# Kernel tuning notes

Hardware: AMD Instinct MI355X
Metric: run time of the kernel (lower is better)

## Reference

```python
import jax, jax.numpy as jnp
import numpy as np

B, LQ, LK, D = 16, 1024, 4096, 256
SQRT_SCALE_INV = 0.25          # D ** -0.25, so scale = 1/sqrt(D)
HALF_BW = 128 // 2             # stripe_bandwdith // 2
NEG_INF = float('-inf')


def setup_inputs() -> dict:
    key = jax.random.key(0)
    k1, k2, k3, k4 = jax.random.split(key, 4)
    query = jax.random.normal(k1, (B, LQ, D), jnp.float32)
    key_t = jax.random.normal(k2, (B, LK, D), jnp.float32)
    value = jax.random.normal(k3, (B, LK, D), jnp.float32)
    # key lengths in [LK//2, LK]; masked_fill in torch requires max == LK
    key_lengths = jax.random.randint(k4, (B,), LK // 2, LK + 1).astype(jnp.int32)
    key_lengths = key_lengths.at[0].set(LK)
    query_lengths = jnp.full((B,), LQ, dtype=jnp.int32)  # full so no all-masked rows
    mask = jnp.arange(LK)[None, :] < key_lengths[:, None]  # [B, LK] bool, True = valid
    return {"query": query, "key": key_t, "value": value, "mask": mask,
            "query_lengths": query_lengths, "key_lengths": key_lengths}


def _stripe_mask(query_lengths, key_lengths, Lq, Lk):
    # band around line y = x * (key_len / query_len), per sample
    gx = jnp.arange(Lq, dtype=jnp.float32)[None, :, None]   # [1,Lq,1]
    gy = jnp.arange(Lk, dtype=jnp.float32)[None, None, :]   # [1,1,Lk]
    slope = (key_lengths.astype(jnp.float32) /
             query_lengths.astype(jnp.float32))[:, None, None]  # [B,1,1]
    center = gx * slope
    return (gy >= center - HALF_BW) & (gy <= center + HALF_BW)  # [B,Lq,Lk] bool


def reference(query, key, value, mask, query_lengths, key_lengths):
    # scores = (q * s) @ (k * s)^T  ==  (q @ k^T) * s^2
    scores = jnp.einsum('bqd,bkd->bqk', query, key) * (SQRT_SCALE_INV * SQRT_SCALE_INV)
    stripe = _stripe_mask(query_lengths, key_lengths, query.shape[1], key.shape[1])
    full_mask = mask[:, None, :] & stripe                    # padding AND stripe
    scores = jnp.where(full_mask, scores.astype(jnp.float32), NEG_INF)
    weight = jax.nn.softmax(scores, axis=-1).astype(query.dtype)
    # module applies no dropout (p=0) and returns (attn_weight, value)
    return (weight, value)
```

## Files before the change

kernel.cpp:

```cpp
#include <hip/hip_runtime.h>
#include <math.h>

constexpr int B_  = 16;
constexpr int LQ_ = 1024;
constexpr int LK_ = 4096;
constexpr int D_  = 256;
constexpr float HALF_BW_F = 64.0f;
constexpr float SCALE = 0.0625f;

typedef float  fx4    __attribute__((ext_vector_type(4)));
typedef short  bf16x8 __attribute__((ext_vector_type(8)));
typedef float  f32x4v __attribute__((ext_vector_type(4)));

constexpr int ROWS_PER_WAVE = 16;
constexpr int ROWS_PER_BLK  = 64;
constexpr int NUNIT = (B_ * LQ_) / ROWS_PER_BLK;
constexpr int NXCD  = 8;
constexpr int UNIT_PER_XCD = NUNIT / NXCD;
constexpr int KSPAN = 192;
constexpr int NT    = 12;

__device__ __forceinline__ unsigned short f2bf(float f) {
    unsigned int u = __float_as_uint(f);
    return (unsigned short)((u + 0x7FFFu + ((u >> 16) & 1u)) >> 16);
}
__device__ __forceinline__ bf16x8 pack8(float4 a, float4 b) {
    bf16x8 r;
    r[0] = (short)f2bf(a.x); r[1] = (short)f2bf(a.y);
    r[2] = (short)f2bf(a.z); r[3] = (short)f2bf(a.w);
    r[4] = (short)f2bf(b.x); r[5] = (short)f2bf(b.y);
    r[6] = (short)f2bf(b.z); r[7] = (short)f2bf(b.w);
    return r;
}
__device__ __forceinline__ float grp16_max(float v) {
    #pragma unroll
    for (int off = 8; off > 0; off >>= 1)
        v = fmaxf(v, __shfl_xor(v, off, 64));
    return v;
}
__device__ __forceinline__ float grp16_sum(float v) {
    #pragma unroll
    for (int off = 8; off > 0; off >>= 1)
        v += __shfl_xor(v, off, 64);
    return v;
}

__global__ __launch_bounds__(256, 2) void stripe_attn_kernel(
    const float* __restrict__ Q, const float* __restrict__ K,
    const float* __restrict__ V,
    const int* __restrict__ qlen, const int* __restrict__ klen,
    float* __restrict__ Wout, float* __restrict__ Vout)
{
    const int Bid  = blockIdx.x;
    const int xcd  = Bid & 7;
    const int type = (Bid >> 3) & 1;
    const int slot = Bid >> 4;
    const int cu_u = xcd * UNIT_PER_XCD + slot;
    const int tid  = threadIdx.x;
    const int lane = tid & 63;
    const int wave = tid >> 6;
    const int row0 = cu_u * ROWS_PER_BLK + wave * ROWS_PER_WAVE;
    const int b    = row0 >> 10;
    const int qi0  = row0 & (LQ_ - 1);

    const int   key_len = klen[b];
    const float slope   = (float)key_len / (float)qlen[b];

    if (type == 1) {
        const float* vs = V    + (size_t)row0 * 1024;
        float*       vd = Vout + (size_t)row0 * 1024;
        #pragma unroll
        for (int it = 0; it < 64; ++it) {
            const int o = (it * 64 + lane) * 4;
            fx4 t = __builtin_nontemporal_load((const fx4*)(vs + o));
            __builtin_nontemporal_store(t, (fx4*)(vd + o));
        }
        const fx4 z4 = {0.f, 0.f, 0.f, 0.f};
        #pragma unroll
        for (int r = 0; r < 16; ++r) {
            const float center = (float)(qi0 + r) * slope;
            int lo = (int)ceilf(center - HALF_BW_F); if (lo < 0) lo = 0;
            int hi = (int)floorf(center + HALF_BW_F); if (hi > key_len - 1) hi = key_len - 1;
            const int s_lo = lo >> 8, s_hi = hi >> 8;
            float* base = Wout + (size_t)(row0 + r) * LK_;
            #pragma unroll
            for (int j = 0; j < 16; ++j) {
                if (j < s_lo || j > s_hi)
                    __builtin_nontemporal_store(z4, (fx4*)(base + (j * 64 + lane) * 4));
            }
        }
        return;
    }

    __shared__ float s_sc[4][ROWS_PER_WAVE][KSPAN];

    int lo_w = (int)ceilf((float)qi0 * slope - HALF_BW_F);
    if (lo_w < 0) lo_w = 0;
    int hi_w = (int)floorf((float)(qi0 + 15) * slope + HALF_BW_F);
    if (hi_w > key_len - 1) hi_w = key_len - 1;
    const int nt = (hi_w - lo_w) / 16 + 1;

    const int col = lane & 15;
    const int kg  = lane >> 4;

    const float* qb = Q + ((size_t)b * LQ_ + qi0 + col) * D_ + kg * 8;
    bf16x8 qf[8];
    #pragma unroll
    for (int kc = 0; kc < 8; ++kc) {
        const float4 u = *(const float4*)(qb + kc * 32);
        const float4 v = *(const float4*)(qb + kc * 32 + 4);
        qf[kc] = pack8(u, v);
    }

    const float* kb = K + (size_t)b * LK_ * D_ + kg * 8;
    f32x4v acc[NT];
    #pragma unroll
    for (int t = 0; t < NT; ++t) acc[t] = (f32x4v){0.f, 0.f, 0.f, 0.f};

    #pragma unroll
    for (int t = 0; t < NT; ++t) {
        if (t < nt) {
            const int key  = lo_w + t * 16 + col;
            const int keyc = (key <= hi_w) ? key : hi_w;
            const float* kp = kb + (size_t)keyc * D_;
            float4 u[8], w[8];
            #pragma unroll
            for (int kc = 0; kc < 8; ++kc) {
                u[kc] = *(const float4*)(kp + kc * 32);
                w[kc] = *(const float4*)(kp + kc * 32 + 4);
            }
            #pragma unroll
            for (int kc = 0; kc < 8; ++kc) {
                const bf16x8 kf = pack8(u[kc], w[kc]);
                acc[t] = __builtin_amdgcn_mfma_f32_16x16x32_bf16(qf[kc], kf, acc[t], 0, 0, 0);
            }
        }
    }

    #pragma unroll
    for (int r = 0; r < 4; ++r) {
        const int rg = kg * 4 + r;
        const float center = (float)(qi0 + rg) * slope;
        int klo = (int)ceilf(center - HALF_BW_F); if (klo < 0) klo = 0;
        int khi = (int)floorf(center + HALF_BW_F); if (khi > key_len - 1) khi = key_len - 1;

        float v[NT];
        #pragma unroll
        for (int t = 0; t < NT; ++t) {
            const int key = lo_w + t * 16 + col;
            v[t] = (t < nt && key >= klo && key <= khi) ? acc[t][r] * SCALE : -INFINITY;
        }
        float mx = v[0];
        #pragma unroll
        for (int t = 1; t < NT; ++t) mx = fmaxf(mx, v[t]);
        mx = grp16_max(mx);

        float e[NT], ssum = 0.f;
        #pragma unroll
        for (int t = 0; t < NT; ++t) { e[t] = __expf(v[t] - mx); ssum += e[t]; }
        ssum = grp16_sum(ssum);
        const float inv = 1.0f / ssum;

        #pragma unroll
        for (int t = 0; t < NT; ++t)
            if (t < nt) s_sc[wave][rg][t * 16 + col] = e[t] * inv;
    }

    #pragma unroll
    for (int r = 0; r < 16; ++r) {
        const float center = (float)(qi0 + r) * slope;
        int klo = (int)ceilf(center - HALF_BW_F); if (klo < 0) klo = 0;
        int khi = (int)floorf(center + HALF_BW_F); if (khi > key_len - 1) khi = key_len - 1;
        const int s_lo = klo >> 8, s_hi = khi >> 8;
        float* base = Wout + (size_t)(row0 + r) * LK_;
        const float* sr = &s_sc[wave][r][0];
        for (int j = s_lo; j <= s_hi; ++j) {
            const int c0 = (j * 64 + lane) * 4;
            float w[4] = {0.f, 0.f, 0.f, 0.f};
            if (c0 + 3 >= klo && c0 <= khi) {
                #pragma unroll
                for (int i = 0; i < 4; ++i) {
                    const int c = c0 + i;
                    if (c >= klo && c <= khi) w[i] = sr[c - lo_w];
                }
            }
            fx4 w4; w4.x = w[0]; w4.y = w[1]; w4.z = w[2]; w4.w = w[3];
            __builtin_nontemporal_store(w4, (fx4*)(base + c0));
        }
    }
}

extern "C" void kernel_launch(void* const* d_in, const int* in_sizes, int n_in,
                              void* d_out, int out_size, void* d_ws, size_t ws_size,
                              hipStream_t stream) {
    const float* Q    = (const float*)d_in[0];
    const float* K    = (const float*)d_in[1];
    const float* V    = (const float*)d_in[2];
    const int*   qlen = (const int*)d_in[4];
    const int*   klen = (const int*)d_in[5];

    float* Wout = (float*)d_out;
    const size_t W_ELEMS = (size_t)B_ * LQ_ * LK_;
    float* Vout = Wout + W_ELEMS;

    stripe_attn_kernel<<<dim3(2 * NUNIT), dim3(256), 0, stream>>>(
        Q, K, V, qlen, klen, Wout, Vout);
}
```

Baseline: 102.6 us.

## Split zero-fill and value copy into memset/memcpy, shrink score kernel to one wave

Removes the fused zero-fill and value-copy path from the kernel. The weight matrix is now cleared with hipMemsetAsync and value is copied with hipMemcpyAsync, followed by a one-wave-per-block score kernel that writes only the band tiles with ordinary stores. This uses the runtime's optimized fill and copy engines and simplifies the kernel, but the whole 256 MB weight matrix is now written twice (memset, then band overwrite) instead of once. It also adds serialized launches on the stream.

```diff
diff --git a/kernel.cpp b/kernel.cpp
--- a/kernel.cpp
+++ b/kernel.cpp
@@ -8,13 +8,11 @@
 constexpr float HALF_BW_F = 64.0f;
 constexpr float SCALE = 0.0625f;
 
-typedef float  fx4    __attribute__((ext_vector_type(4)));
 typedef short  bf16x8 __attribute__((ext_vector_type(8)));
 typedef float  f32x4v __attribute__((ext_vector_type(4)));
 
 constexpr int ROWS_PER_WAVE = 16;
-constexpr int ROWS_PER_BLK  = 64;
-constexpr int NUNIT = (B_ * LQ_) / ROWS_PER_BLK;
+constexpr int NUNIT = (B_ * LQ_) / ROWS_PER_WAVE;
 constexpr int NXCD  = 8;
 constexpr int UNIT_PER_XCD = NUNIT / NXCD;
 constexpr int KSPAN = 192;
@@ -45,54 +43,22 @@
     return v;
 }
 
-__global__ __launch_bounds__(256, 2) void stripe_attn_kernel(
+__global__ __launch_bounds__(64, 2) void score_kernel(
     const float* __restrict__ Q, const float* __restrict__ K,
-    const float* __restrict__ V,
     const int* __restrict__ qlen, const int* __restrict__ klen,
-    float* __restrict__ Wout, float* __restrict__ Vout)
+    float* __restrict__ Wout)
 {
     const int Bid  = blockIdx.x;
-    const int xcd  = Bid & 7;
-    const int type = (Bid >> 3) & 1;
-    const int slot = Bid >> 4;
-    const int cu_u = xcd * UNIT_PER_XCD + slot;
-    const int tid  = threadIdx.x;
-    const int lane = tid & 63;
-    const int wave = tid >> 6;
-    const int row0 = cu_u * ROWS_PER_BLK + wave * ROWS_PER_WAVE;
+    const int rb   = (Bid & (NXCD - 1)) * UNIT_PER_XCD + (Bid >> 3);
+    const int lane = threadIdx.x;
+    const int row0 = rb * ROWS_PER_WAVE;
     const int b    = row0 >> 10;
     const int qi0  = row0 & (LQ_ - 1);
 
+    __shared__ float s_sc[ROWS_PER_WAVE][KSPAN];
+
     const int   key_len = klen[b];
     const float slope   = (float)key_len / (float)qlen[b];
-
-    if (type == 1) {
-        const float* vs = V    + (size_t)row0 * 1024;
-        float*       vd = Vout + (size_t)row0 * 1024;
-        #pragma unroll
-        for (int it = 0; it < 64; ++it) {
-            const int o = (it * 64 + lane) * 4;
-            fx4 t = __builtin_nontemporal_load((const fx4*)(vs + o));
-            __builtin_nontemporal_store(t, (fx4*)(vd + o));
-        }
-        const fx4 z4 = {0.f, 0.f, 0.f, 0.f};
-        #pragma unroll
-        for (int r = 0; r < 16; ++r) {
-            const float center = (float)(qi0 + r) * slope;
-            int lo = (int)ceilf(center - HALF_BW_F); if (lo < 0) lo = 0;
-            int hi = (int)floorf(center + HALF_BW_F); if (hi > key_len - 1) hi = key_len - 1;
-            const int s_lo = lo >> 8, s_hi = hi >> 8;
-            float* base = Wout + (size_t)(row0 + r) * LK_;
-            #pragma unroll
-            for (int j = 0; j < 16; ++j) {
-                if (j < s_lo || j > s_hi)
-                    __builtin_nontemporal_store(z4, (fx4*)(base + (j * 64 + lane) * 4));
-            }
-        }
-        return;
-    }
-
-    __shared__ float s_sc[4][ROWS_PER_WAVE][KSPAN];
 
     int lo_w = (int)ceilf((float)qi0 * slope - HALF_BW_F);
     if (lo_w < 0) lo_w = 0;
@@ -163,7 +129,7 @@
 
         #pragma unroll
         for (int t = 0; t < NT; ++t)
-            if (t < nt) s_sc[wave][rg][t * 16 + col] = e[t] * inv;
+            if (t < nt) s_sc[rg][t * 16 + col] = e[t] * inv;
     }
 
     #pragma unroll
@@ -173,7 +139,7 @@
         int khi = (int)floorf(center + HALF_BW_F); if (khi > key_len - 1) khi = key_len - 1;
         const int s_lo = klo >> 8, s_hi = khi >> 8;
         float* base = Wout + (size_t)(row0 + r) * LK_;
-        const float* sr = &s_sc[wave][r][0];
+        const float* sr = &s_sc[r][0];
         for (int j = s_lo; j <= s_hi; ++j) {
             const int c0 = (j * 64 + lane) * 4;
             float w[4] = {0.f, 0.f, 0.f, 0.f};
@@ -184,8 +150,8 @@
                     if (c >= klo && c <= khi) w[i] = sr[c - lo_w];
                 }
             }
-            fx4 w4; w4.x = w[0]; w4.y = w[1]; w4.z = w[2]; w4.w = w[3];
-            __builtin_nontemporal_store(w4, (fx4*)(base + c0));
+            float4 w4; w4.x = w[0]; w4.y = w[1]; w4.z = w[2]; w4.w = w[3];
+            *(float4*)(base + c0) = w4;
         }
     }
 }
@@ -202,7 +168,10 @@
     float* Wout = (float*)d_out;
     const size_t W_ELEMS = (size_t)B_ * LQ_ * LK_;
     float* Vout = Wout + W_ELEMS;
+    const size_t W_BYTES = W_ELEMS * sizeof(float);
+    const size_t V_BYTES = (size_t)B_ * LK_ * D_ * sizeof(float);
 
-    stripe_attn_kernel<<<dim3(2 * NUNIT), dim3(256), 0, stream>>>(
-        Q, K, V, qlen, klen, Wout, Vout);
+    hipMemsetAsync(Wout, 0, W_BYTES, stream);
+    hipMemcpyAsync(Vout, V, V_BYTES, hipMemcpyDeviceToDevice, stream);
+    score_kernel<<<dim3(NUNIT), dim3(64), 0, stream>>>(Q, K, qlen, klen, Wout);
 }
```

Result: slower. 141.3 us (+37.8%).
